# Kernel optimization log

Hardware: AMD Instinct MI355X
Metric: run time of the kernel (lower is better)

Reference implementation:

```python
import jax, jax.numpy as jnp
import numpy as np

H = 1024
V = 50257
S = 2048


def setup_inputs() -> dict:
    key = jax.random.key(0)
    ks = jax.random.split(key, 16)
    sc = 0.05
    return {
        "input_ids": jax.random.randint(ks[0], (1,), 0, V, dtype=jnp.int64)
        if jax.config.jax_enable_x64
        else jax.random.randint(ks[0], (1,), 0, V, dtype=jnp.int32),
        "h0": jax.random.normal(ks[1], (1, 1, H), dtype=jnp.float32),
        "c0": jax.random.normal(ks[2], (1, 1, H), dtype=jnp.float32),
        "encoder_hiddens": jax.random.normal(ks[3], (1, S, H), dtype=jnp.float32),
        "embedding": jax.random.normal(ks[4], (V, H), dtype=jnp.float32) * sc,
        "attn_W": jax.random.normal(ks[5], (1, 2 * H), dtype=jnp.float32) * sc,
        "attn_b": jax.random.normal(ks[6], (1,), dtype=jnp.float32) * sc,
        "comb_W": jax.random.normal(ks[7], (H, 2 * H), dtype=jnp.float32) * sc,
        "comb_b": jax.random.normal(ks[8], (H,), dtype=jnp.float32) * sc,
        "W_ih": jax.random.normal(ks[9], (4 * H, H), dtype=jnp.float32) * sc,
        "W_hh": jax.random.normal(ks[10], (4 * H, H), dtype=jnp.float32) * sc,
        "b_ih": jax.random.normal(ks[11], (4 * H,), dtype=jnp.float32) * sc,
        "b_hh": jax.random.normal(ks[12], (4 * H,), dtype=jnp.float32) * sc,
        "out_W": jax.random.normal(ks[13], (V, H), dtype=jnp.float32) * sc,
        "out_b": jax.random.normal(ks[14], (V,), dtype=jnp.float32) * sc,
    }


def reference(input_ids, h0, c0, encoder_hiddens, embedding, attn_W, attn_b,
              comb_W, comb_b, W_ih, W_hh, b_ih, b_hh, out_W, out_b):
    x = embedding[input_ids[0]]          # [H] embedded token
    h = h0[0, 0]                          # [H]
    c = c0[0, 0]                          # [H]
    enc = encoder_hiddens[0]              # [S, H]

    # attention: linear score per position (NO softmax in original), then
    # context = enc^T @ coeff
    hiddens = jnp.concatenate([enc, jnp.broadcast_to(h, enc.shape)], axis=1)  # [S, 2H]
    coeff = hiddens @ attn_W.T + attn_b   # [S, 1]
    context = (enc.T @ coeff)[:, 0]       # [H]

    combined = jnp.concatenate([x, context]) @ comb_W.T + comb_b  # [H]
    z = jax.nn.relu(combined)

    # single LSTM step, PyTorch gate order i, f, g, o
    gates = W_ih @ z + b_ih + W_hh @ h + b_hh  # [4H]
    i, f, g, o = jnp.split(gates, 4)
    i = jax.nn.sigmoid(i)
    f = jax.nn.sigmoid(f)
    g = jnp.tanh(g)
    o = jax.nn.sigmoid(o)
    c_new = f * c + i * g
    h_new = o * jnp.tanh(c_new)

    logits = h_new @ out_W.T + out_b      # [V]
    logp = jax.nn.log_softmax(logits)[None, :]  # [1, V]
    return logp, h_new[None, None, :], c_new[None, None, :]
```

## Files before the change

kernel.cpp:

```cpp
#include <hip/hip_runtime.h>
#include <math.h>

#define H 1024
#define V 50257
#define S 2048
#define NCH 64
#define LB 6283

#define O_CTXP   0
#define O_Z      65536
#define O_HNEW   66560
#define O_PART   67584
#define O_LOGITS 80152

__device__ inline float wred_sum(float v) {
    for (int o = 32; o > 0; o >>= 1) v += __shfl_down(v, o, 64);
    return v;
}
__device__ inline float sigm(float x) { return 1.f / (1.f + expf(-x)); }

__global__ __launch_bounds__(256) void k_attn(const float* __restrict__ enc,
        const float* __restrict__ h0, const float* __restrict__ attn_W,
        const float* __restrict__ attn_b, float* __restrict__ ws) {
    const int ch = blockIdx.x, t = threadIdx.x, lane = t & 63, wave = t >> 6;
    __shared__ float scoef[32];
    __shared__ float sred[4];

    float4 hv = ((const float4*)h0)[t];
    float4 wv = ((const float4*)(attn_W + H))[t];
    float p = hv.x*wv.x + hv.y*wv.y + hv.z*wv.z + hv.w*wv.w;
    p = wred_sum(p);
    if (lane == 0) sred[wave] = p;
    __syncthreads();
    const float hdot = sred[0] + sred[1] + sred[2] + sred[3] + attn_b[0];

    const float4* w0 = (const float4*)attn_W;
    const int s0 = ch * 32;
    for (int r = 0; r < 8; ++r) {
        int s = s0 + wave * 8 + r;
        const float4* e4 = (const float4*)(enc + (size_t)s * H);
        float acc = 0.f;
        #pragma unroll
        for (int kk = 0; kk < 4; ++kk) {
            float4 e = e4[kk*64 + lane], w = w0[kk*64 + lane];
            acc += e.x*w.x + e.y*w.y + e.z*w.z + e.w*w.w;
        }
        acc = wred_sum(acc);
        if (lane == 0) scoef[wave * 8 + r] = acc + hdot;
    }
    __syncthreads();

    float4 a4 = make_float4(0.f, 0.f, 0.f, 0.f);
    for (int r = 0; r < 32; ++r) {
        float c = scoef[r];
        float4 e = ((const float4*)(enc + (size_t)(s0 + r) * H))[t];
        a4.x += c * e.x; a4.y += c * e.y; a4.z += c * e.z; a4.w += c * e.w;
    }
    ((float4*)(ws + O_CTXP + ch * H))[t] = a4;
}

__global__ __launch_bounds__(256) void k_z(const float* __restrict__ emb,
        const int* __restrict__ ids, const float* __restrict__ comb_W,
        const float* __restrict__ comb_b, float* __restrict__ ws) {
    const int b = blockIdx.x, t = threadIdx.x, lane = t & 63, wave = t >> 6;
    __shared__ __align__(16) float sctx[H];
    float4 a4 = make_float4(0.f, 0.f, 0.f, 0.f);
    #pragma unroll 8
    for (int ch = 0; ch < NCH; ++ch) {
        float4 v = ((const float4*)(ws + O_CTXP + ch * H))[t];
        a4.x += v.x; a4.y += v.y; a4.z += v.z; a4.w += v.w;
    }
    ((float4*)sctx)[t] = a4;
    __syncthreads();

    const int tok = ids[0];
    const int i = b * 4 + wave;
    const float4* wrow = (const float4*)(comb_W + (size_t)i * 2 * H);
    const float4* x4 = (const float4*)(emb + (size_t)tok * H);
    const float4* c4 = (const float4*)sctx;
    float acc = 0.f;
    #pragma unroll
    for (int kk = 0; kk < 4; ++kk) {
        int k4 = kk * 64 + lane;
        float4 w = wrow[k4], a = x4[k4];
        acc += w.x*a.x + w.y*a.y + w.z*a.z + w.w*a.w;
        float4 w2 = wrow[256 + k4], a2 = c4[k4];
        acc += w2.x*a2.x + w2.y*a2.y + w2.z*a2.z + w2.w*a2.w;
    }
    acc = wred_sum(acc);
    if (lane == 0) ws[O_Z + i] = fmaxf(acc + comb_b[i], 0.f);
}

__global__ __launch_bounds__(256) void k_gates_lstm(const float* __restrict__ W_ih,
        const float* __restrict__ W_hh, const float* __restrict__ b_ih,
        const float* __restrict__ b_hh, const float* __restrict__ h0,
        const float* __restrict__ c0, float* __restrict__ ws, float* __restrict__ out) {
    const int j = blockIdx.x, t = threadIdx.x, lane = t & 63, g = t >> 6;
    __shared__ float sg[4];
    const int row = g * H + j;
    const float4* wi = (const float4*)(W_ih + (size_t)row * H);
    const float4* wh = (const float4*)(W_hh + (size_t)row * H);
    const float4* zv = (const float4*)(ws + O_Z);
    const float4* hv = (const float4*)h0;
    float acc = 0.f;
    #pragma unroll
    for (int kk = 0; kk < 4; ++kk) {
        int k4 = kk * 64 + lane;
        float4 a = wi[k4], z4 = zv[k4];
        acc += a.x*z4.x + a.y*z4.y + a.z*z4.z + a.w*z4.w;
        float4 c2 = wh[k4], h4 = hv[k4];
        acc += c2.x*h4.x + c2.y*h4.y + c2.z*h4.z + c2.w*h4.w;
    }
    acc = wred_sum(acc);
    if (lane == 0) sg[g] = acc + b_ih[row] + b_hh[row];
    __syncthreads();
    if (t == 0) {
        float ig = sigm(sg[0]);
        float fg = sigm(sg[1]);
        float gg = tanhf(sg[2]);
        float og = sigm(sg[3]);
        float cn = fg * c0[j] + ig * gg;
        float hn = og * tanhf(cn);
        out[V + j]     = hn;
        out[V + H + j] = cn;
        ws[O_HNEW + j] = hn;
    }
}

__global__ __launch_bounds__(512) void k_logits(const float* __restrict__ out_W,
        const float* __restrict__ out_b, float* __restrict__ ws) {
    const int t = threadIdx.x, lane = t & 63, w8 = t >> 6;
    const int v = blockIdx.x * 8 + w8;
    __shared__ float slg[8];
    const float4* hv = (const float4*)(ws + O_HNEW);
    float acc = 0.f;
    if (v < V) {
        const float4* wr = (const float4*)(out_W + (size_t)v * H);
        #pragma unroll
        for (int kk = 0; kk < 4; ++kk) {
            int k4 = kk * 64 + lane;
            float4 w = wr[k4], a = hv[k4];
            acc += w.x*a.x + w.y*a.y + w.z*a.z + w.w*a.w;
        }
    }
    acc = wred_sum(acc);
    if (lane == 0) {
        if (v < V) {
            float lg = acc + out_b[v];
            ws[O_LOGITS + v] = lg;
            slg[w8] = lg;
        } else {
            slg[w8] = -1e30f;
        }
    }
    __syncthreads();
    if (t == 0) {
        float m = slg[0];
        #pragma unroll
        for (int i = 1; i < 8; ++i) m = fmaxf(m, slg[i]);
        float s = 0.f;
        #pragma unroll
        for (int i = 0; i < 8; ++i) s += expf(slg[i] - m);
        ws[O_PART + 2 * blockIdx.x]     = m;
        ws[O_PART + 2 * blockIdx.x + 1] = s;
    }
}

__global__ __launch_bounds__(1024) void k_logp(const float* __restrict__ ws,
        float* __restrict__ out) {
    const int t = threadIdx.x, lane = t & 63, wv = t >> 6;
    __shared__ float smm[16], sss[16];
    __shared__ float slse;
    float m = -1e30f, s = 0.f;
    for (int i = t; i < LB; i += 1024) {
        float m2 = ws[O_PART + 2 * i], s2 = ws[O_PART + 2 * i + 1];
        float M = fmaxf(m, m2);
        s = s * expf(m - M) + s2 * expf(m2 - M);
        m = M;
    }
    for (int o = 32; o > 0; o >>= 1) {
        float m2 = __shfl_down(m, o, 64), s2 = __shfl_down(s, o, 64);
        float M = fmaxf(m, m2);
        s = s * expf(m - M) + s2 * expf(m2 - M);
        m = M;
    }
    if (lane == 0) { smm[wv] = m; sss[wv] = s; }
    __syncthreads();
    if (t == 0) {
        float M = smm[0], Ssum = sss[0];
        #pragma unroll
        for (int i = 1; i < 16; ++i) {
            float MM = fmaxf(M, smm[i]);
            Ssum = Ssum * expf(M - MM) + sss[i] * expf(smm[i] - MM);
            M = MM;
        }
        slse = M + logf(Ssum);
    }
    __syncthreads();
    const float lse = slse;
    int v = blockIdx.x * 1024 + t;
    if (v < V) out[v] = ws[O_LOGITS + v] - lse;
}

extern "C" void kernel_launch(void* const* d_in, const int* in_sizes, int n_in,
                              void* d_out, int out_size, void* d_ws, size_t ws_size,
                              hipStream_t stream) {
    const int*   ids    = (const int*)  d_in[0];
    const float* h0     = (const float*)d_in[1];
    const float* c0     = (const float*)d_in[2];
    const float* enc    = (const float*)d_in[3];
    const float* emb    = (const float*)d_in[4];
    const float* attn_W = (const float*)d_in[5];
    const float* attn_b = (const float*)d_in[6];
    const float* comb_W = (const float*)d_in[7];
    const float* comb_b = (const float*)d_in[8];
    const float* W_ih   = (const float*)d_in[9];
    const float* W_hh   = (const float*)d_in[10];
    const float* b_ih   = (const float*)d_in[11];
    const float* b_hh   = (const float*)d_in[12];
    const float* out_W  = (const float*)d_in[13];
    const float* out_b  = (const float*)d_in[14];
    float* out = (float*)d_out;
    float* ws  = (float*)d_ws;

    k_attn      <<<NCH, 256, 0, stream>>>(enc, h0, attn_W, attn_b, ws);
    k_z         <<<256, 256, 0, stream>>>(emb, ids, comb_W, comb_b, ws);
    k_gates_lstm<<<1024, 256, 0, stream>>>(W_ih, W_hh, b_ih, b_hh, h0, c0, ws, out);
    k_logits    <<<LB, 512, 0, stream>>>(out_W, out_b, ws);
    k_logp      <<<64, 1024, 0, stream>>>(ws, out);
}
```

Measured before the change: 66.36 us.

## Fuse attention, combine, LSTM and logits into one persistent kernel with atomic barriers

Replaces four separate launches with a single kernel. Work is assigned by ticket order, and the stages are chained through global atomic counters with spin-waits, so launch gaps vanish and later blocks can start loading out_W while earlier stages finish. The context reduction becomes a parallel stage instead of every k_z block summing 64 partials, and LSTM and logits blocks each compute two rows per wave. This relies on blocks that hold early tickets making progress while others spin. That is a deadlock risk if scheduling is unfavorable, and the spinning adds contention.

New measurement: 221.3 us. 234% more time.

```diff
diff --git a/kernel.cpp b/kernel.cpp
--- a/kernel.cpp
+++ b/kernel.cpp
@@ -5,164 +5,224 @@
 #define V 50257
 #define S 2048
 #define NCH 64
-#define LB 6283
+#define GRID 6283
+#define TPRE 512
 
 #define O_CTXP   0
-#define O_Z      65536
-#define O_HNEW   66560
-#define O_PART   67584
-#define O_LOGITS 80152
+#define O_CTX    65536
+#define O_Z      66560
+#define O_HNEW   67584
+#define O_PART   68608
+#define O_LOGITS 81174
+
+__device__ unsigned g_ticket;
+__device__ unsigned g_sync[64];
 
 __device__ inline float wred_sum(float v) {
     for (int o = 32; o > 0; o >>= 1) v += __shfl_down(v, o, 64);
     return v;
 }
 __device__ inline float sigm(float x) { return 1.f / (1.f + expf(-x)); }
-
-__global__ __launch_bounds__(256) void k_attn(const float* __restrict__ enc,
-        const float* __restrict__ h0, const float* __restrict__ attn_W,
-        const float* __restrict__ attn_b, float* __restrict__ ws) {
-    const int ch = blockIdx.x, t = threadIdx.x, lane = t & 63, wave = t >> 6;
+__device__ inline float dot4(float4 a, float4 b) {
+    return a.x*b.x + a.y*b.y + a.z*b.z + a.w*b.w;
+}
+
+__device__ inline void sig(unsigned* c) {
+    __syncthreads();
+    if (threadIdx.x == 0) {
+        __threadfence();
+        __hip_atomic_fetch_add(c, 1u, __ATOMIC_RELEASE, __HIP_MEMORY_SCOPE_AGENT);
+    }
+}
+template<int SLP>
+__device__ inline void waitc(unsigned* c, unsigned target) {
+    if (threadIdx.x == 0) {
+        while ((int)(__hip_atomic_load(c, __ATOMIC_RELAXED, __HIP_MEMORY_SCOPE_AGENT) - target) < 0)
+            __builtin_amdgcn_s_sleep(SLP);
+        __builtin_amdgcn_fence(__ATOMIC_ACQUIRE, "agent");
+    }
+    __syncthreads();
+}
+
+__global__ __launch_bounds__(256, 4) void mega(
+    const int* __restrict__ ids, const float* __restrict__ h0,
+    const float* __restrict__ c0, const float* __restrict__ enc,
+    const float* __restrict__ emb, const float* __restrict__ attn_W,
+    const float* __restrict__ attn_b, const float* __restrict__ comb_W,
+    const float* __restrict__ comb_b, const float* __restrict__ W_ih,
+    const float* __restrict__ W_hh, const float* __restrict__ b_ih,
+    const float* __restrict__ b_hh, const float* __restrict__ out_W,
+    const float* __restrict__ out_b, float* __restrict__ out,
+    float* __restrict__ ws)
+{
+    const int t = threadIdx.x, lane = t & 63, wave = t >> 6;
+    __shared__ unsigned stk;
+    __shared__ float sred[8];
     __shared__ float scoef[32];
-    __shared__ float sred[4];
-
-    float4 hv = ((const float4*)h0)[t];
-    float4 wv = ((const float4*)(attn_W + H))[t];
-    float p = hv.x*wv.x + hv.y*wv.y + hv.z*wv.z + hv.w*wv.w;
-    p = wred_sum(p);
-    if (lane == 0) sred[wave] = p;
-    __syncthreads();
-    const float hdot = sred[0] + sred[1] + sred[2] + sred[3] + attn_b[0];
-
-    const float4* w0 = (const float4*)attn_W;
-    const int s0 = ch * 32;
-    for (int r = 0; r < 8; ++r) {
-        int s = s0 + wave * 8 + r;
-        const float4* e4 = (const float4*)(enc + (size_t)s * H);
+    __shared__ float slg[8];
+
+    if (t == 0)
+        stk = __hip_atomic_fetch_add(&g_ticket, 1u, __ATOMIC_RELAXED,
+                                     __HIP_MEMORY_SCOPE_AGENT);
+    __syncthreads();
+    const unsigned tg = stk;
+    const unsigned r  = tg / GRID;
+    const unsigned tk = tg - r * GRID;
+    unsigned* cA  = &g_sync[0];
+    unsigned* cA2 = &g_sync[16];
+    unsigned* cB  = &g_sync[32];
+    unsigned* cC  = &g_sync[48];
+
+    if (tk < NCH) {
+        float4 hv4 = ((const float4*)h0)[t];
+        float4 wv4 = ((const float4*)(attn_W + H))[t];
+        float p = wred_sum(dot4(hv4, wv4));
+        if (lane == 0) sred[wave] = p;
+        __syncthreads();
+        const float hdot = sred[0] + sred[1] + sred[2] + sred[3] + attn_b[0];
+        const float4* w0 = (const float4*)attn_W;
+        const int s0 = tk * 32;
+        #pragma unroll
+        for (int gq = 0; gq < 2; ++gq) {
+            int sb = s0 + wave * 8 + gq * 4;
+            const float4* e0 = (const float4*)(enc + (size_t)(sb    ) * H);
+            const float4* e1 = (const float4*)(enc + (size_t)(sb + 1) * H);
+            const float4* e2 = (const float4*)(enc + (size_t)(sb + 2) * H);
+            const float4* e3 = (const float4*)(enc + (size_t)(sb + 3) * H);
+            float a0 = 0.f, a1 = 0.f, a2 = 0.f, a3 = 0.f;
+            #pragma unroll
+            for (int kk = 0; kk < 4; ++kk) {
+                int k4 = kk * 64 + lane;
+                float4 w = w0[k4];
+                a0 += dot4(e0[k4], w); a1 += dot4(e1[k4], w);
+                a2 += dot4(e2[k4], w); a3 += dot4(e3[k4], w);
+            }
+            a0 = wred_sum(a0); a1 = wred_sum(a1);
+            a2 = wred_sum(a2); a3 = wred_sum(a3);
+            if (lane == 0) {
+                scoef[wave*8 + gq*4 + 0] = a0 + hdot;
+                scoef[wave*8 + gq*4 + 1] = a1 + hdot;
+                scoef[wave*8 + gq*4 + 2] = a2 + hdot;
+                scoef[wave*8 + gq*4 + 3] = a3 + hdot;
+            }
+        }
+        __syncthreads();
+        float4 a4 = make_float4(0.f, 0.f, 0.f, 0.f);
+        #pragma unroll 8
+        for (int rr = 0; rr < 32; ++rr) {
+            float c = scoef[rr];
+            float4 e = ((const float4*)(enc + (size_t)(s0 + rr) * H))[t];
+            a4.x += c * e.x; a4.y += c * e.y; a4.z += c * e.z; a4.w += c * e.w;
+        }
+        ((float4*)(ws + O_CTXP + tk * H))[t] = a4;
+        sig(cA);
+        waitc<4>(cA, r * NCH + NCH);
+        #pragma unroll
+        for (int q = 0; q < 4; ++q) {
+            int j = tk * 16 + wave * 4 + q;
+            float v = wred_sum(ws[O_CTXP + lane * H + j]);
+            if (lane == 0) ws[O_CTX + j] = v;
+        }
+        sig(cA2);
+    }
+    if (tk < 256) {
+        waitc<4>(cA2, r * NCH + NCH);
+        const int tok = ids[0];
+        const int i = tk * 4 + wave;
+        const float4* wrow = (const float4*)(comb_W + (size_t)i * 2 * H);
+        const float4* x4 = (const float4*)(emb + (size_t)tok * H);
+        const float4* c4 = (const float4*)(ws + O_CTX);
         float acc = 0.f;
-        #pragma unroll
-        for (int kk = 0; kk < 4; ++kk) {
-            float4 e = e4[kk*64 + lane], w = w0[kk*64 + lane];
-            acc += e.x*w.x + e.y*w.y + e.z*w.z + e.w*w.w;
-        }
-        acc = wred_sum(acc);
-        if (lane == 0) scoef[wave * 8 + r] = acc + hdot;
-    }
-    __syncthreads();
-
-    float4 a4 = make_float4(0.f, 0.f, 0.f, 0.f);
-    for (int r = 0; r < 32; ++r) {
-        float c = scoef[r];
-        float4 e = ((const float4*)(enc + (size_t)(s0 + r) * H))[t];
-        a4.x += c * e.x; a4.y += c * e.y; a4.z += c * e.z; a4.w += c * e.w;
-    }
-    ((float4*)(ws + O_CTXP + ch * H))[t] = a4;
-}
-
-__global__ __launch_bounds__(256) void k_z(const float* __restrict__ emb,
-        const int* __restrict__ ids, const float* __restrict__ comb_W,
-        const float* __restrict__ comb_b, float* __restrict__ ws) {
-    const int b = blockIdx.x, t = threadIdx.x, lane = t & 63, wave = t >> 6;
-    __shared__ __align__(16) float sctx[H];
-    float4 a4 = make_float4(0.f, 0.f, 0.f, 0.f);
-    #pragma unroll 8
-    for (int ch = 0; ch < NCH; ++ch) {
-        float4 v = ((const float4*)(ws + O_CTXP + ch * H))[t];
-        a4.x += v.x; a4.y += v.y; a4.z += v.z; a4.w += v.w;
-    }
-    ((float4*)sctx)[t] = a4;
-    __syncthreads();
-
-    const int tok = ids[0];
-    const int i = b * 4 + wave;
-    const float4* wrow = (const float4*)(comb_W + (size_t)i * 2 * H);
-    const float4* x4 = (const float4*)(emb + (size_t)tok * H);
-    const float4* c4 = (const float4*)sctx;
-    float acc = 0.f;
-    #pragma unroll
-    for (int kk = 0; kk < 4; ++kk) {
-        int k4 = kk * 64 + lane;
-        float4 w = wrow[k4], a = x4[k4];
-        acc += w.x*a.x + w.y*a.y + w.z*a.z + w.w*a.w;
-        float4 w2 = wrow[256 + k4], a2 = c4[k4];
-        acc += w2.x*a2.x + w2.y*a2.y + w2.z*a2.z + w2.w*a2.w;
-    }
-    acc = wred_sum(acc);
-    if (lane == 0) ws[O_Z + i] = fmaxf(acc + comb_b[i], 0.f);
-}
-
-__global__ __launch_bounds__(256) void k_gates_lstm(const float* __restrict__ W_ih,
-        const float* __restrict__ W_hh, const float* __restrict__ b_ih,
-        const float* __restrict__ b_hh, const float* __restrict__ h0,
-        const float* __restrict__ c0, float* __restrict__ ws, float* __restrict__ out) {
-    const int j = blockIdx.x, t = threadIdx.x, lane = t & 63, g = t >> 6;
-    __shared__ float sg[4];
-    const int row = g * H + j;
-    const float4* wi = (const float4*)(W_ih + (size_t)row * H);
-    const float4* wh = (const float4*)(W_hh + (size_t)row * H);
-    const float4* zv = (const float4*)(ws + O_Z);
-    const float4* hv = (const float4*)h0;
-    float acc = 0.f;
-    #pragma unroll
-    for (int kk = 0; kk < 4; ++kk) {
-        int k4 = kk * 64 + lane;
-        float4 a = wi[k4], z4 = zv[k4];
-        acc += a.x*z4.x + a.y*z4.y + a.z*z4.z + a.w*z4.w;
-        float4 c2 = wh[k4], h4 = hv[k4];
-        acc += c2.x*h4.x + c2.y*h4.y + c2.z*h4.z + c2.w*h4.w;
-    }
-    acc = wred_sum(acc);
-    if (lane == 0) sg[g] = acc + b_ih[row] + b_hh[row];
-    __syncthreads();
-    if (t == 0) {
-        float ig = sigm(sg[0]);
-        float fg = sigm(sg[1]);
-        float gg = tanhf(sg[2]);
-        float og = sigm(sg[3]);
-        float cn = fg * c0[j] + ig * gg;
-        float hn = og * tanhf(cn);
-        out[V + j]     = hn;
-        out[V + H + j] = cn;
-        ws[O_HNEW + j] = hn;
-    }
-}
-
-__global__ __launch_bounds__(512) void k_logits(const float* __restrict__ out_W,
-        const float* __restrict__ out_b, float* __restrict__ ws) {
-    const int t = threadIdx.x, lane = t & 63, w8 = t >> 6;
-    const int v = blockIdx.x * 8 + w8;
-    __shared__ float slg[8];
-    const float4* hv = (const float4*)(ws + O_HNEW);
-    float acc = 0.f;
-    if (v < V) {
-        const float4* wr = (const float4*)(out_W + (size_t)v * H);
         #pragma unroll
         for (int kk = 0; kk < 4; ++kk) {
             int k4 = kk * 64 + lane;
-            float4 w = wr[k4], a = hv[k4];
-            acc += w.x*a.x + w.y*a.y + w.z*a.z + w.w*a.w;
-        }
-    }
-    acc = wred_sum(acc);
-    if (lane == 0) {
-        if (v < V) {
-            float lg = acc + out_b[v];
-            ws[O_LOGITS + v] = lg;
-            slg[w8] = lg;
-        } else {
-            slg[w8] = -1e30f;
-        }
-    }
-    __syncthreads();
-    if (t == 0) {
-        float m = slg[0];
-        #pragma unroll
-        for (int i = 1; i < 8; ++i) m = fmaxf(m, slg[i]);
-        float s = 0.f;
-        #pragma unroll
-        for (int i = 0; i < 8; ++i) s += expf(slg[i] - m);
-        ws[O_PART + 2 * blockIdx.x]     = m;
-        ws[O_PART + 2 * blockIdx.x + 1] = s;
+            acc += dot4(wrow[k4], x4[k4]);
+            acc += dot4(wrow[256 + k4], c4[k4]);
+        }
+        acc = wred_sum(acc);
+        if (lane == 0) ws[O_Z + i] = fmaxf(acc + comb_b[i], 0.f);
+        sig(cB);
+    }
+    if (tk < TPRE) {
+        waitc<4>(cB, r * 256 + 256);
+        const int j0 = tk * 2;
+        const int row0 = wave * H + j0, row1 = row0 + 1;
+        const float4* wi0 = (const float4*)(W_ih + (size_t)row0 * H);
+        const float4* wi1 = (const float4*)(W_ih + (size_t)row1 * H);
+        const float4* wh0 = (const float4*)(W_hh + (size_t)row0 * H);
+        const float4* wh1 = (const float4*)(W_hh + (size_t)row1 * H);
+        const float4* zv = (const float4*)(ws + O_Z);
+        const float4* hv = (const float4*)h0;
+        float acc0 = 0.f, acc1 = 0.f;
+        #pragma unroll
+        for (int kk = 0; kk < 4; ++kk) {
+            int k4 = kk * 64 + lane;
+            float4 z4 = zv[k4], h4 = hv[k4];
+            acc0 += dot4(wi0[k4], z4) + dot4(wh0[k4], h4);
+            acc1 += dot4(wi1[k4], z4) + dot4(wh1[k4], h4);
+        }
+        acc0 = wred_sum(acc0); acc1 = wred_sum(acc1);
+        if (lane == 0) {
+            sred[wave * 2    ] = acc0 + b_ih[row0] + b_hh[row0];
+            sred[wave * 2 + 1] = acc1 + b_ih[row1] + b_hh[row1];
+        }
+        __syncthreads();
+        if (t < 2) {
+            int j = j0 + t;
+            float ig = sigm(sred[0 + t]);
+            float fg = sigm(sred[2 + t]);
+            float gg = tanhf(sred[4 + t]);
+            float og = sigm(sred[6 + t]);
+            float cn = fg * c0[j] + ig * gg;
+            float hn = og * tanhf(cn);
+            out[V + j]     = hn;
+            out[V + H + j] = cn;
+            ws[O_HNEW + j] = hn;
+        }
+        sig(cC);
+        waitc<4>(cC, r * TPRE + TPRE);
+    } else {
+        waitc<64>(cC, r * TPRE + TPRE);
+    }
+
+    {
+        const float4* hv = (const float4*)(ws + O_HNEW);
+        float4 hr[4];
+        #pragma unroll
+        for (int kk = 0; kk < 4; ++kk) hr[kk] = hv[kk * 64 + lane];
+        const int v0 = blockIdx.x * 8 + wave * 2;
+        const int v1 = v0 + 1;
+        const bool q0 = v0 < V, q1 = v1 < V;
+        const float4* w0r = (const float4*)(out_W + (size_t)(q0 ? v0 : 0) * H);
+        const float4* w1r = (const float4*)(out_W + (size_t)(q1 ? v1 : 0) * H);
+        float acc0 = 0.f, acc1 = 0.f;
+        #pragma unroll
+        for (int kk = 0; kk < 4; ++kk) {
+            int k4 = kk * 64 + lane;
+            float4 a = hr[kk];
+            acc0 += dot4(w0r[k4], a);
+            acc1 += dot4(w1r[k4], a);
+        }
+        acc0 = wred_sum(acc0); acc1 = wred_sum(acc1);
+        if (lane == 0) {
+            float l0 = acc0 + out_b[q0 ? v0 : 0];
+            float l1 = acc1 + out_b[q1 ? v1 : 0];
+            if (q0) ws[O_LOGITS + v0] = l0;
+            if (q1) ws[O_LOGITS + v1] = l1;
+            slg[wave * 2    ] = q0 ? l0 : -1e30f;
+            slg[wave * 2 + 1] = q1 ? l1 : -1e30f;
+        }
+        __syncthreads();
+        if (t == 0) {
+            float m = slg[0];
+            #pragma unroll
+            for (int i = 1; i < 8; ++i) m = fmaxf(m, slg[i]);
+            float s2 = 0.f;
+            #pragma unroll
+            for (int i = 0; i < 8; ++i) s2 += expf(slg[i] - m);
+            ws[O_PART + 2 * blockIdx.x]     = m;
+            ws[O_PART + 2 * blockIdx.x + 1] = s2;
+        }
     }
 }
 
@@ -172,7 +232,7 @@
     __shared__ float smm[16], sss[16];
     __shared__ float slse;
     float m = -1e30f, s = 0.f;
-    for (int i = t; i < LB; i += 1024) {
+    for (int i = t; i < GRID; i += 1024) {
         float m2 = ws[O_PART + 2 * i], s2 = ws[O_PART + 2 * i + 1];
         float M = fmaxf(m, m2);
         s = s * expf(m - M) + s2 * expf(m2 - M);
@@ -223,9 +283,8 @@
     float* out = (float*)d_out;
     float* ws  = (float*)d_ws;
 
-    k_attn      <<<NCH, 256, 0, stream>>>(enc, h0, attn_W, attn_b, ws);
-    k_z         <<<256, 256, 0, stream>>>(emb, ids, comb_W, comb_b, ws);
-    k_gates_lstm<<<1024, 256, 0, stream>>>(W_ih, W_hh, b_ih, b_hh, h0, c0, ws, out);
-    k_logits    <<<LB, 512, 0, stream>>>(out_W, out_b, ws);
-    k_logp      <<<64, 1024, 0, stream>>>(ws, out);
-}
+    mega  <<<GRID, 256, 0, stream>>>(ids, h0, c0, enc, emb, attn_W, attn_b,
+                                     comb_W, comb_b, W_ih, W_hh, b_ih, b_hh,
+                                     out_W, out_b, out, ws);
+    k_logp<<<64, 1024, 0, stream>>>(ws, out);
+}
```

## Overlap W_hh gate matvec with attention and split context reduction

Applied to the files above, without the earlier changes.

The W_hh·h0 gate pre-activation, which does not depend on the attention result, is moved into the attention kernel as extra blocks so it runs alongside the encoder scoring, and the later gate kernel only streams W_ih. Attention now uses 128 chunks of 16 rows, with four rows per wave sharing each weight load. A separate k_ctx kernel reduces the context partials once, so the 256 k_z blocks no longer each repeat that sum. k_logits computes four vocab rows per wave and writes logits directly into the output buffer, and k_logp subtracts the log-sum-exp in place, removing the workspace logits copy. This adds one extra launch in exchange.

Measured after the change: 71.58 us. 7.9% more time.

```diff
diff --git a/kernel.cpp b/kernel.cpp
--- a/kernel.cpp
+++ b/kernel.cpp
@@ -4,115 +4,157 @@
 #define H 1024
 #define V 50257
 #define S 2048
-#define NCH 64
-#define LB 6283
+#define NCH 128
+#define NPART 3142
 
 #define O_CTXP   0
-#define O_Z      65536
-#define O_HNEW   66560
-#define O_PART   67584
-#define O_LOGITS 80152
+#define O_CTX    131072
+#define O_Z      132096
+#define O_GPRE   133120
+#define O_HNEW   137216
+#define O_PART   138240
 
 __device__ inline float wred_sum(float v) {
     for (int o = 32; o > 0; o >>= 1) v += __shfl_down(v, o, 64);
     return v;
 }
 __device__ inline float sigm(float x) { return 1.f / (1.f + expf(-x)); }
+__device__ inline float dot4(float4 a, float4 b) {
+    return a.x*b.x + a.y*b.y + a.z*b.z + a.w*b.w;
+}
 
 __global__ __launch_bounds__(256) void k_attn(const float* __restrict__ enc,
         const float* __restrict__ h0, const float* __restrict__ attn_W,
-        const float* __restrict__ attn_b, float* __restrict__ ws) {
-    const int ch = blockIdx.x, t = threadIdx.x, lane = t & 63, wave = t >> 6;
-    __shared__ float scoef[32];
-    __shared__ float sred[4];
-
-    float4 hv = ((const float4*)h0)[t];
-    float4 wv = ((const float4*)(attn_W + H))[t];
-    float p = hv.x*wv.x + hv.y*wv.y + hv.z*wv.z + hv.w*wv.w;
-    p = wred_sum(p);
-    if (lane == 0) sred[wave] = p;
-    __syncthreads();
-    const float hdot = sred[0] + sred[1] + sred[2] + sred[3] + attn_b[0];
-
-    const float4* w0 = (const float4*)attn_W;
-    const int s0 = ch * 32;
-    for (int r = 0; r < 8; ++r) {
-        int s = s0 + wave * 8 + r;
-        const float4* e4 = (const float4*)(enc + (size_t)s * H);
-        float acc = 0.f;
+        const float* __restrict__ attn_b, const float* __restrict__ W_hh,
+        const float* __restrict__ b_ih, const float* __restrict__ b_hh,
+        float* __restrict__ ws) {
+    const int b = blockIdx.x, t = threadIdx.x, lane = t & 63, wave = t >> 6;
+    if (b < NCH) {
+        __shared__ float sred[4];
+        __shared__ float scoef[16];
+        float4 hv4 = ((const float4*)h0)[t];
+        float4 wv4 = ((const float4*)(attn_W + H))[t];
+        float p = wred_sum(dot4(hv4, wv4));
+        if (lane == 0) sred[wave] = p;
+        __syncthreads();
+        const float hdot = sred[0] + sred[1] + sred[2] + sred[3] + attn_b[0];
+        const float4* w0 = (const float4*)attn_W;
+        const int s0 = b * 16;
+        {
+            int sb = s0 + wave * 4;
+            const float4* e0 = (const float4*)(enc + (size_t)(sb    ) * H);
+            const float4* e1 = (const float4*)(enc + (size_t)(sb + 1) * H);
+            const float4* e2 = (const float4*)(enc + (size_t)(sb + 2) * H);
+            const float4* e3 = (const float4*)(enc + (size_t)(sb + 3) * H);
+            float a0 = 0.f, a1 = 0.f, a2 = 0.f, a3 = 0.f;
+            #pragma unroll
+            for (int kk = 0; kk < 4; ++kk) {
+                int k4 = kk * 64 + lane;
+                float4 w = w0[k4];
+                a0 += dot4(e0[k4], w); a1 += dot4(e1[k4], w);
+                a2 += dot4(e2[k4], w); a3 += dot4(e3[k4], w);
+            }
+            a0 = wred_sum(a0); a1 = wred_sum(a1);
+            a2 = wred_sum(a2); a3 = wred_sum(a3);
+            if (lane == 0) {
+                scoef[wave*4 + 0] = a0 + hdot;
+                scoef[wave*4 + 1] = a1 + hdot;
+                scoef[wave*4 + 2] = a2 + hdot;
+                scoef[wave*4 + 3] = a3 + hdot;
+            }
+        }
+        __syncthreads();
+        float4 a4 = make_float4(0.f, 0.f, 0.f, 0.f);
+        #pragma unroll 4
+        for (int rr = 0; rr < 16; ++rr) {
+            float c = scoef[rr];
+            float4 e = ((const float4*)(enc + (size_t)(s0 + rr) * H))[t];
+            a4.x += c * e.x; a4.y += c * e.y; a4.z += c * e.z; a4.w += c * e.w;
+        }
+        ((float4*)(ws + O_CTXP + b * H))[t] = a4;
+    } else {
+        const int bb = b - NCH;
+        float4 hr[4];
+        #pragma unroll
+        for (int kk = 0; kk < 4; ++kk) hr[kk] = ((const float4*)h0)[kk*64 + lane];
+        const int r0 = bb * 16 + wave * 4;
+        const float4* m0 = (const float4*)(W_hh + (size_t)(r0    ) * H);
+        const float4* m1 = (const float4*)(W_hh + (size_t)(r0 + 1) * H);
+        const float4* m2 = (const float4*)(W_hh + (size_t)(r0 + 2) * H);
+        const float4* m3 = (const float4*)(W_hh + (size_t)(r0 + 3) * H);
+        float a0 = 0.f, a1 = 0.f, a2 = 0.f, a3 = 0.f;
         #pragma unroll
         for (int kk = 0; kk < 4; ++kk) {
-            float4 e = e4[kk*64 + lane], w = w0[kk*64 + lane];
-            acc += e.x*w.x + e.y*w.y + e.z*w.z + e.w*w.w;
-        }
-        acc = wred_sum(acc);
-        if (lane == 0) scoef[wave * 8 + r] = acc + hdot;
-    }
-    __syncthreads();
-
-    float4 a4 = make_float4(0.f, 0.f, 0.f, 0.f);
-    for (int r = 0; r < 32; ++r) {
-        float c = scoef[r];
-        float4 e = ((const float4*)(enc + (size_t)(s0 + r) * H))[t];
-        a4.x += c * e.x; a4.y += c * e.y; a4.z += c * e.z; a4.w += c * e.w;
-    }
-    ((float4*)(ws + O_CTXP + ch * H))[t] = a4;
+            int k4 = kk * 64 + lane;
+            float4 a = hr[kk];
+            a0 += dot4(m0[k4], a); a1 += dot4(m1[k4], a);
+            a2 += dot4(m2[k4], a); a3 += dot4(m3[k4], a);
+        }
+        a0 = wred_sum(a0); a1 = wred_sum(a1);
+        a2 = wred_sum(a2); a3 = wred_sum(a3);
+        if (lane == 0) {
+            ws[O_GPRE + r0    ] = a0 + b_ih[r0    ] + b_hh[r0    ];
+            ws[O_GPRE + r0 + 1] = a1 + b_ih[r0 + 1] + b_hh[r0 + 1];
+            ws[O_GPRE + r0 + 2] = a2 + b_ih[r0 + 2] + b_hh[r0 + 2];
+            ws[O_GPRE + r0 + 3] = a3 + b_ih[r0 + 3] + b_hh[r0 + 3];
+        }
+    }
+}
+
+__global__ __launch_bounds__(256) void k_ctx(float* __restrict__ ws) {
+    const int b = blockIdx.x, t = threadIdx.x;
+    const int jj = t & 15, cg = t >> 4;
+    const int j0 = b * 16;
+    float acc = 0.f;
+    #pragma unroll
+    for (int k = 0; k < 8; ++k)
+        acc += ws[O_CTXP + (size_t)(cg + 16*k) * H + j0 + jj];
+    __shared__ float sarr[256];
+    sarr[t] = acc;
+    __syncthreads();
+    if (t < 16) {
+        float a = 0.f;
+        #pragma unroll
+        for (int g = 0; g < 16; ++g) a += sarr[g * 16 + t];
+        ws[O_CTX + j0 + t] = a;
+    }
 }
 
 __global__ __launch_bounds__(256) void k_z(const float* __restrict__ emb,
         const int* __restrict__ ids, const float* __restrict__ comb_W,
         const float* __restrict__ comb_b, float* __restrict__ ws) {
     const int b = blockIdx.x, t = threadIdx.x, lane = t & 63, wave = t >> 6;
-    __shared__ __align__(16) float sctx[H];
-    float4 a4 = make_float4(0.f, 0.f, 0.f, 0.f);
-    #pragma unroll 8
-    for (int ch = 0; ch < NCH; ++ch) {
-        float4 v = ((const float4*)(ws + O_CTXP + ch * H))[t];
-        a4.x += v.x; a4.y += v.y; a4.z += v.z; a4.w += v.w;
-    }
-    ((float4*)sctx)[t] = a4;
-    __syncthreads();
-
     const int tok = ids[0];
     const int i = b * 4 + wave;
     const float4* wrow = (const float4*)(comb_W + (size_t)i * 2 * H);
     const float4* x4 = (const float4*)(emb + (size_t)tok * H);
-    const float4* c4 = (const float4*)sctx;
+    const float4* c4 = (const float4*)(ws + O_CTX);
     float acc = 0.f;
     #pragma unroll
     for (int kk = 0; kk < 4; ++kk) {
         int k4 = kk * 64 + lane;
-        float4 w = wrow[k4], a = x4[k4];
-        acc += w.x*a.x + w.y*a.y + w.z*a.z + w.w*a.w;
-        float4 w2 = wrow[256 + k4], a2 = c4[k4];
-        acc += w2.x*a2.x + w2.y*a2.y + w2.z*a2.z + w2.w*a2.w;
+        acc += dot4(wrow[k4], x4[k4]);
+        acc += dot4(wrow[256 + k4], c4[k4]);
     }
     acc = wred_sum(acc);
     if (lane == 0) ws[O_Z + i] = fmaxf(acc + comb_b[i], 0.f);
 }
 
 __global__ __launch_bounds__(256) void k_gates_lstm(const float* __restrict__ W_ih,
-        const float* __restrict__ W_hh, const float* __restrict__ b_ih,
-        const float* __restrict__ b_hh, const float* __restrict__ h0,
         const float* __restrict__ c0, float* __restrict__ ws, float* __restrict__ out) {
     const int j = blockIdx.x, t = threadIdx.x, lane = t & 63, g = t >> 6;
     __shared__ float sg[4];
     const int row = g * H + j;
     const float4* wi = (const float4*)(W_ih + (size_t)row * H);
-    const float4* wh = (const float4*)(W_hh + (size_t)row * H);
     const float4* zv = (const float4*)(ws + O_Z);
-    const float4* hv = (const float4*)h0;
     float acc = 0.f;
     #pragma unroll
     for (int kk = 0; kk < 4; ++kk) {
         int k4 = kk * 64 + lane;
-        float4 a = wi[k4], z4 = zv[k4];
-        acc += a.x*z4.x + a.y*z4.y + a.z*z4.z + a.w*z4.w;
-        float4 c2 = wh[k4], h4 = hv[k4];
-        acc += c2.x*h4.x + c2.y*h4.y + c2.z*h4.z + c2.w*h4.w;
+        acc += dot4(wi[k4], zv[k4]);
     }
     acc = wred_sum(acc);
-    if (lane == 0) sg[g] = acc + b_ih[row] + b_hh[row];
+    if (lane == 0) sg[g] = acc + ws[O_GPRE + row];
     __syncthreads();
     if (t == 0) {
         float ig = sigm(sg[0]);
@@ -127,40 +169,53 @@
     }
 }
 
-__global__ __launch_bounds__(512) void k_logits(const float* __restrict__ out_W,
-        const float* __restrict__ out_b, float* __restrict__ ws) {
-    const int t = threadIdx.x, lane = t & 63, w8 = t >> 6;
-    const int v = blockIdx.x * 8 + w8;
-    __shared__ float slg[8];
+__global__ __launch_bounds__(256) void k_logits(const float* __restrict__ out_W,
+        const float* __restrict__ out_b, float* __restrict__ ws,
+        float* __restrict__ out) {
+    const int t = threadIdx.x, lane = t & 63, wave = t >> 6;
+    __shared__ float slg[16];
     const float4* hv = (const float4*)(ws + O_HNEW);
-    float acc = 0.f;
-    if (v < V) {
-        const float4* wr = (const float4*)(out_W + (size_t)v * H);
-        #pragma unroll
-        for (int kk = 0; kk < 4; ++kk) {
-            int k4 = kk * 64 + lane;
-            float4 w = wr[k4], a = hv[k4];
-            acc += w.x*a.x + w.y*a.y + w.z*a.z + w.w*a.w;
-        }
-    }
-    acc = wred_sum(acc);
+    float4 hr[4];
+    #pragma unroll
+    for (int kk = 0; kk < 4; ++kk) hr[kk] = hv[kk * 64 + lane];
+    const int v0 = blockIdx.x * 16 + wave * 4;
+    const bool q0 = v0 < V, q1 = v0 + 1 < V, q2 = v0 + 2 < V, q3 = v0 + 3 < V;
+    const float4* w0 = (const float4*)(out_W + (size_t)(q0 ? v0     : 0) * H);
+    const float4* w1 = (const float4*)(out_W + (size_t)(q1 ? v0 + 1 : 0) * H);
+    const float4* w2 = (const float4*)(out_W + (size_t)(q2 ? v0 + 2 : 0) * H);
+    const float4* w3 = (const float4*)(out_W + (size_t)(q3 ? v0 + 3 : 0) * H);
+    float a0 = 0.f, a1 = 0.f, a2 = 0.f, a3 = 0.f;
+    #pragma unroll
+    for (int kk = 0; kk < 4; ++kk) {
+        int k4 = kk * 64 + lane;
+        float4 a = hr[kk];
+        a0 += dot4(w0[k4], a); a1 += dot4(w1[k4], a);
+        a2 += dot4(w2[k4], a); a3 += dot4(w3[k4], a);
+    }
+    a0 = wred_sum(a0); a1 = wred_sum(a1);
+    a2 = wred_sum(a2); a3 = wred_sum(a3);
     if (lane == 0) {
-        if (v < V) {
-            float lg = acc + out_b[v];
-            ws[O_LOGITS + v] = lg;
-            slg[w8] = lg;
-        } else {
-            slg[w8] = -1e30f;
-        }
+        float l0 = a0 + out_b[q0 ? v0     : 0];
+        float l1 = a1 + out_b[q1 ? v0 + 1 : 0];
+        float l2 = a2 + out_b[q2 ? v0 + 2 : 0];
+        float l3 = a3 + out_b[q3 ? v0 + 3 : 0];
+        if (q0) out[v0    ] = l0;
+        if (q1) out[v0 + 1] = l1;
+        if (q2) out[v0 + 2] = l2;
+        if (q3) out[v0 + 3] = l3;
+        slg[wave*4 + 0] = q0 ? l0 : -1e30f;
+        slg[wave*4 + 1] = q1 ? l1 : -1e30f;
+        slg[wave*4 + 2] = q2 ? l2 : -1e30f;
+        slg[wave*4 + 3] = q3 ? l3 : -1e30f;
     }
     __syncthreads();
     if (t == 0) {
         float m = slg[0];
         #pragma unroll
-        for (int i = 1; i < 8; ++i) m = fmaxf(m, slg[i]);
+        for (int i = 1; i < 16; ++i) m = fmaxf(m, slg[i]);
         float s = 0.f;
         #pragma unroll
-        for (int i = 0; i < 8; ++i) s += expf(slg[i] - m);
+        for (int i = 0; i < 16; ++i) s += expf(slg[i] - m);
         ws[O_PART + 2 * blockIdx.x]     = m;
         ws[O_PART + 2 * blockIdx.x + 1] = s;
     }
@@ -172,7 +227,7 @@
     __shared__ float smm[16], sss[16];
     __shared__ float slse;
     float m = -1e30f, s = 0.f;
-    for (int i = t; i < LB; i += 1024) {
+    for (int i = t; i < NPART; i += 1024) {
         float m2 = ws[O_PART + 2 * i], s2 = ws[O_PART + 2 * i + 1];
         float M = fmaxf(m, m2);
         s = s * expf(m - M) + s2 * expf(m2 - M);
@@ -198,8 +253,8 @@
     }
     __syncthreads();
     const float lse = slse;
-    int v = blockIdx.x * 1024 + t;
-    if (v < V) out[v] = ws[O_LOGITS + v] - lse;
+    const int v = blockIdx.x * 1024 + t;
+    if (v < V) out[v] = out[v] - lse;
 }
 
 extern "C" void kernel_launch(void* const* d_in, const int* in_sizes, int n_in,
@@ -223,9 +278,11 @@
     float* out = (float*)d_out;
     float* ws  = (float*)d_ws;
 
-    k_attn      <<<NCH, 256, 0, stream>>>(enc, h0, attn_W, attn_b, ws);
+    k_attn      <<<NCH + 256, 256, 0, stream>>>(enc, h0, attn_W, attn_b,
+                                                W_hh, b_ih, b_hh, ws);
+    k_ctx       <<<64, 256, 0, stream>>>(ws);
     k_z         <<<256, 256, 0, stream>>>(emb, ids, comb_W, comb_b, ws);
-    k_gates_lstm<<<1024, 256, 0, stream>>>(W_ih, W_hh, b_ih, b_hh, h0, c0, ws, out);
-    k_logits    <<<LB, 512, 0, stream>>>(out_W, out_b, ws);
+    k_gates_lstm<<<1024, 256, 0, stream>>>(W_ih, c0, ws, out);
+    k_logits    <<<NPART, 256, 0, stream>>>(out_W, out_b, ws, out);
     k_logp      <<<64, 1024, 0, stream>>>(ws, out);
 }
```
